# Kernel optimization log

Hardware: AMD Instinct MI355X
Metric: run time of the kernel (lower is better)

Reference implementation:

```python
import jax, jax.numpy as jnp
import numpy as np

B, T, D, H, E, K = 4, 2048, 512, 1024, 8, 2


def setup_inputs() -> dict:
    key = jax.random.key(0)
    ks = jax.random.split(key, 6)
    x = jax.random.normal(ks[0], (B, T, D), dtype=jnp.float32)
    Wg = jax.random.normal(ks[1], (D, E), dtype=jnp.float32) / np.sqrt(D)  # gate (no bias)
    W1 = jax.random.normal(ks[2], (E, D, H), dtype=jnp.float32) / np.sqrt(D)
    b1 = jnp.zeros((E, H), dtype=jnp.float32)
    W2 = jax.random.normal(ks[3], (E, H, D), dtype=jnp.float32) / np.sqrt(H)
    b2 = jnp.zeros((E, D), dtype=jnp.float32)
    return {"x": x, "Wg": Wg, "W1": W1, "b1": b1, "W2": W2, "b2": b2}


def reference(x, Wg, W1, b1, W2, b2):
    # Dropout is identity at inference (p applied only in train mode).
    Bx, Tx, Dx = x.shape
    N = Bx * Tx
    xf = x.reshape(N, Dx)

    # --- Router: top-k over gate logits, softmax over the k selected logits ---
    router_logits = xf @ Wg                               # [N, E]
    topk_logits, topk_idx = jax.lax.top_k(router_logits, K)  # [N, K]
    topk_w = jax.nn.softmax(topk_logits, axis=-1)         # [N, K]

    # Dense combine weights: combine[n, e] = sum of topk weights routing token n to expert e
    combine = jnp.zeros((N, E), dtype=x.dtype).at[
        jnp.arange(N)[:, None], topk_idx
    ].add(topk_w)                                         # [N, E]

    # --- Experts (batched over E): GELU(x W1 + b1) W2 + b2 ---
    h = jax.nn.gelu(jnp.einsum('nd,edh->enh', xf, W1) + b1[:, None, :],
                    approximate=False)                    # [E, N, H]
    y = jnp.einsum('enh,ehd->end', h, W2) + b2[:, None, :]  # [E, N, D]

    # --- Combine: weighted sum of expert outputs per token ---
    out = jnp.einsum('end,ne->nd', y, combine).reshape(Bx, Tx, Dx)

    aux_logits = router_logits.reshape(Bx, Tx, E)
    aux_idx = topk_idx.reshape(Bx, Tx, K)
    aux_w = topk_w.reshape(Bx, Tx, K)
    return out, aux_logits, aux_idx, aux_w
```

## Files before the change

### kernel.cpp

```cpp
#include <hip/hip_runtime.h>
#include <hip/hip_bf16.h>

#define NTOK 8192
#define DDIM 512
#define HDIM 1024
#define NEXP 8
#define TOPK 2

typedef __attribute__((ext_vector_type(8))) short short8;
typedef __attribute__((ext_vector_type(4))) float f32x4;

__device__ __forceinline__ short f2bf(float f) {
  union { float f; unsigned u; } v; v.f = f;
  unsigned r = v.u + 0x7fffu + ((v.u >> 16) & 1u);
  return (short)(r >> 16);
}
__device__ __forceinline__ float bf2f(short s) {
  union { unsigned u; float f; } v; v.u = ((unsigned)(unsigned short)s) << 16;
  return v.f;
}

__device__ __forceinline__ void async_lds16(const void* g, void* l) {
  __builtin_amdgcn_global_load_lds(
      (const __attribute__((address_space(1))) unsigned int*)g,
      (__attribute__((address_space(3))) unsigned int*)l,
      16, 0, 0);
}

__device__ __forceinline__ float gelu_f(float v) {
  float u2 = v * v;
  float z = v * (-1.5957691216f - 0.0713548163f * u2);
  float t = __expf(z);
  return v * __builtin_amdgcn_rcpf(1.f + t);
}

__global__ __launch_bounds__(256) void prep_kernel(
    const float* __restrict__ w1, short* __restrict__ w1t,
    const float* __restrict__ w2, short* __restrict__ w2t,
    const float* __restrict__ x, const float* __restrict__ wg,
    float* __restrict__ out_logits, float* __restrict__ out_idx,
    float* __restrict__ out_w, short* __restrict__ xb, int* __restrict__ counts) {
  __shared__ float tile[32][33];
  int raw = blockIdx.x;
  if (raw < 8192) {
    int z = raw >> 9;
    int tile_id = raw & 511;
    int R = (z < 8) ? DDIM : HDIM;
    int C = (z < 8) ? HDIM : DDIM;
    const float* s = ((z < 8) ? w1 : w2) + (size_t)(z & 7) * DDIM * HDIM;
    short* d = ((z < 8) ? w1t : w2t) + (size_t)(z & 7) * DDIM * HDIM;
    int tc = (z < 8) ? (tile_id & 31) : (tile_id & 15);
    int tr = (z < 8) ? (tile_id >> 5) : (tile_id >> 4);
    int c0 = tc * 32, r0 = tr * 32;
    int tx = threadIdx.x & 31, ty = threadIdx.x >> 5;
#pragma unroll
    for (int i = 0; i < 4; ++i)
      tile[ty + i * 8][tx] = s[(size_t)(r0 + ty + i * 8) * C + c0 + tx];
    __syncthreads();
#pragma unroll
    for (int i = 0; i < 4; ++i)
      d[(size_t)(c0 + ty + i * 8) * R + r0 + tx] = f2bf(tile[tx][ty + i * 8]);
    return;
  }
  int rb = raw - 8192;
  if (rb == 0 && threadIdx.x < NEXP) counts[threadIdx.x] = 0;
  int wave = threadIdx.x >> 6;
  int lane = threadIdx.x & 63;
  int n = rb * 4 + wave;

  const float* xrow = x + (size_t)n * DDIM;
  const float4* xv = (const float4*)xrow;
  float4 xa = xv[lane * 2], xbv = xv[lane * 2 + 1];
  float xs[8] = {xa.x, xa.y, xa.z, xa.w, xbv.x, xbv.y, xbv.z, xbv.w};

  short8 xc;
#pragma unroll
  for (int j = 0; j < 8; ++j) xc[j] = f2bf(xs[j]);
  *(short8*)(xb + (size_t)n * DDIM + lane * 8) = xc;

  float acc[8] = {0, 0, 0, 0, 0, 0, 0, 0};
#pragma unroll
  for (int j = 0; j < 8; ++j) {
    const float4* wr = (const float4*)(wg + (size_t)(lane * 8 + j) * NEXP);
    float4 w0 = wr[0], w1v = wr[1];
    float xj = xs[j];
    acc[0] += xj * w0.x; acc[1] += xj * w0.y; acc[2] += xj * w0.z; acc[3] += xj * w0.w;
    acc[4] += xj * w1v.x; acc[5] += xj * w1v.y; acc[6] += xj * w1v.z; acc[7] += xj * w1v.w;
  }
#pragma unroll
  for (int m = 32; m >= 1; m >>= 1) {
#pragma unroll
    for (int e = 0; e < 8; ++e) acc[e] += __shfl_xor(acc[e], m);
  }
  if (lane == 0) {
#pragma unroll
    for (int e = 0; e < 8; ++e) out_logits[(size_t)n * NEXP + e] = acc[e];
    int i1 = 0; float v1 = acc[0];
#pragma unroll
    for (int e = 1; e < 8; ++e) if (acc[e] > v1) { v1 = acc[e]; i1 = e; }
    int i2 = -1; float v2 = -3.4e38f;
#pragma unroll
    for (int e = 0; e < 8; ++e) if (e != i1 && acc[e] > v2) { v2 = acc[e]; i2 = e; }
    float ex = expf(v2 - v1);
    float s = 1.f / (1.f + ex);
    out_idx[n * 2] = (float)i1; out_idx[n * 2 + 1] = (float)i2;
    out_w[n * 2] = s; out_w[n * 2 + 1] = ex * s;
  }
}

__global__ __launch_bounds__(512) void build_lists(
    const float* __restrict__ idxf,
    int* __restrict__ counts, int* __restrict__ tok_list, int* __restrict__ slot_enc) {
  int t = blockIdx.x * 512 + threadIdx.x;
  int lane = threadIdx.x & 63;
  float2 iv = *(const float2*)(idxf + (size_t)t * 2);
  int es[2] = {(int)iv.x, (int)iv.y};
#pragma unroll
  for (int s = 0; s < 2; ++s) {
    int e = es[s];
#pragma unroll
    for (int ex = 0; ex < NEXP; ++ex) {
      unsigned long long m = __ballot(e == ex);
      if (e == ex) {
        int leader = __ffsll(m) - 1;
        int base = 0;
        if (lane == leader) base = atomicAdd(&counts[ex], __popcll(m));
        base = __shfl(base, leader);
        int rank = __popcll(m & ((1ull << lane) - 1ull));
        tok_list[ex * NTOK + base + rank] = t;
        slot_enc[t * 2 + s] = (ex << 16) | (base + rank);
      }
    }
  }
}

__global__ __launch_bounds__(256) void expert_gemm1(
    const short* __restrict__ xb, const short* __restrict__ w1t,
    const float* __restrict__ b1, short* __restrict__ hbuf,
    const int* __restrict__ ctrl, const int* __restrict__ tok_list) {
  int raw = blockIdx.x;
  int bid = (raw & 7) * 512 + (raw >> 3);
  int e = bid >> 9;
  int rem = bid & 511;
  int mt = rem >> 3;
  int nt = rem & 7;
  int ce = ctrl[e];
  int m0 = mt * 128;
  if (m0 >= ce) return;
  int offe = 0;
#pragma unroll
  for (int i = 0; i < NEXP; ++i) offe += (i < e) ? ctrl[i] : 0;

  __shared__ char smem[34816];

  int tid = threadIdx.x;
  int wave = tid >> 6;
  int lane = tid & 63;

  int sr = tid >> 2;
  int kc = (((tid & 3) ^ ((sr >> 1) & 3)) * 8);
  int ia = m0 + sr;      if (ia >= ce) ia = ce - 1;
  int ib = m0 + sr + 64; if (ib >= ce) ib = ce - 1;
  const short* gA0 = xb + (size_t)tok_list[e * NTOK + ia] * DDIM + kc;
  const short* gA1 = xb + (size_t)tok_list[e * NTOK + ib] * DDIM + kc;
  const short* gB0 = w1t + ((size_t)e * HDIM + nt * 128 + sr) * DDIM + kc;
  const short* gB1 = gB0 + (size_t)64 * DDIM;

  f32x4 acc[4][4];
#pragma unroll
  for (int i = 0; i < 4; ++i)
#pragma unroll
    for (int j = 0; j < 4; ++j) acc[i][j] = (f32x4){0.f, 0.f, 0.f, 0.f};

  int wm = (wave >> 1) * 64;
  int wn = (wave & 1) * 64;
  int lr = lane & 15;
  int kswz = ((lane >> 4) * 8) ^ (((lr >> 1) & 3) << 3);

  int colb = nt * 128 + wn;
  float bb[4];
#pragma unroll
  for (int j = 0; j < 4; ++j) bb[j] = b1[e * HDIM + colb + j * 16 + lr];

#define STAGE1(t) do {                                                  \
    int _k = (t) * 32;                                                  \
    char* _lA = smem + (((t) & 1) << 14) + wave * 1024;                 \
    char* _lB = _lA + 8192;                                             \
    async_lds16(gA0 + _k, _lA); async_lds16(gA1 + _k, _lA + 4096);      \
    async_lds16(gB0 + _k, _lB); async_lds16(gB1 + _k, _lB + 4096);      \
  } while (0)

  STAGE1(0);
#pragma unroll
  for (int t = 0; t < 16; ++t) {
    asm volatile("s_waitcnt vmcnt(0)\n\ts_barrier" ::: "memory");
    if (t + 1 < 16) STAGE1(t + 1);
    const short* As = (const short*)(smem + ((t & 1) << 14));
    const short* Bs = As + 4096;
    short8 a[4], b[4];
#pragma unroll
    for (int i = 0; i < 4; ++i) a[i] = *(const short8*)&As[(wm + i * 16 + lr) * 32 + kswz];
#pragma unroll
    for (int j = 0; j < 4; ++j) b[j] = *(const short8*)&Bs[(wn + j * 16 + lr) * 32 + kswz];
    __builtin_amdgcn_s_setprio(1);
#pragma unroll
    for (int i = 0; i < 4; ++i)
#pragma unroll
      for (int j = 0; j < 4; ++j)
        acc[i][j] = __builtin_amdgcn_mfma_f32_16x16x32_bf16(a[i], b[j], acc[i][j], 0, 0, 0);
    __builtin_amdgcn_s_setprio(0);
    asm volatile("s_waitcnt lgkmcnt(0)" ::: "memory");
  }
#undef STAGE1
  __syncthreads();

  short* ep = (short*)(smem + wave * 8704);
#pragma unroll
  for (int j = 0; j < 4; ++j) {
#pragma unroll
    for (int i = 0; i < 4; ++i) {
#pragma unroll
      for (int q = 0; q < 4; ++q) {
        int rl = i * 16 + (lane >> 4) * 4 + q;
        ep[rl * 68 + j * 16 + lr] = f2bf(gelu_f(acc[i][j][q] + bb[j]));
      }
    }
  }
  __syncthreads();
#pragma unroll
  for (int s = 0; s < 8; ++s) {
    int idx = s * 64 + lane;
    int rl = idx >> 3;
    int c8 = (idx & 7) * 8;
    int gidx = m0 + wm + rl;
    if (gidx < ce) {
      *(short8*)&hbuf[(size_t)(offe + gidx) * HDIM + colb + c8] = *(short8*)&ep[rl * 68 + c8];
    }
  }
}

__global__ __launch_bounds__(256) void expert_gemm2(
    const short* __restrict__ hbuf, const short* __restrict__ w2t,
    const float* __restrict__ b2, short* __restrict__ ybuf,
    const int* __restrict__ ctrl) {
  int raw = blockIdx.x;
  int bid = (raw & 7) * 256 + (raw >> 3);
  int e = bid >> 8;
  int rem = bid & 255;
  int mt = rem >> 2;
  int nt = rem & 3;
  int ce = ctrl[e];
  int m0 = mt * 128;
  if (m0 >= ce) return;
  int offe = 0;
#pragma unroll
  for (int i = 0; i < NEXP; ++i) offe += (i < e) ? ctrl[i] : 0;

  __shared__ char smem[34816];

  int tid = threadIdx.x;
  int wave = tid >> 6;
  int lane = tid & 63;

  int sr = tid >> 2;
  int kc = (((tid & 3) ^ ((sr >> 1) & 3)) * 8);
  int ia = m0 + sr;      if (ia >= ce) ia = ce - 1;
  int ib = m0 + sr + 64; if (ib >= ce) ib = ce - 1;
  const short* gA0 = hbuf + (size_t)(offe + ia) * HDIM + kc;
  const short* gA1 = hbuf + (size_t)(offe + ib) * HDIM + kc;
  const short* gB0 = w2t + ((size_t)e * DDIM + nt * 128 + sr) * HDIM + kc;
  const short* gB1 = gB0 + (size_t)64 * HDIM;

  f32x4 acc[4][4];
#pragma unroll
  for (int i = 0; i < 4; ++i)
#pragma unroll
    for (int j = 0; j < 4; ++j) acc[i][j] = (f32x4){0.f, 0.f, 0.f, 0.f};

  int wm = (wave >> 1) * 64;
  int wn = (wave & 1) * 64;
  int lr = lane & 15;
  int kswz = ((lane >> 4) * 8) ^ (((lr >> 1) & 3) << 3);

  int colb = nt * 128 + wn;
  float bb[4];
#pragma unroll
  for (int j = 0; j < 4; ++j) bb[j] = b2[e * DDIM + colb + j * 16 + lr];

#define STAGE2(t) do {                                                  \
    int _k = (t) * 32;                                                  \
    char* _lA = smem + (((t) & 1) << 14) + wave * 1024;                 \
    char* _lB = _lA + 8192;                                             \
    async_lds16(gA0 + _k, _lA); async_lds16(gA1 + _k, _lA + 4096);      \
    async_lds16(gB0 + _k, _lB); async_lds16(gB1 + _k, _lB + 4096);      \
  } while (0)

  STAGE2(0);
#pragma unroll
  for (int t = 0; t < 32; ++t) {
    asm volatile("s_waitcnt vmcnt(0)\n\ts_barrier" ::: "memory");
    if (t + 1 < 32) STAGE2(t + 1);
    const short* As = (const short*)(smem + ((t & 1) << 14));
    const short* Bs = As + 4096;
    short8 a[4], b[4];
#pragma unroll
    for (int i = 0; i < 4; ++i) a[i] = *(const short8*)&As[(wm + i * 16 + lr) * 32 + kswz];
#pragma unroll
    for (int j = 0; j < 4; ++j) b[j] = *(const short8*)&Bs[(wn + j * 16 + lr) * 32 + kswz];
    __builtin_amdgcn_s_setprio(1);
#pragma unroll
    for (int i = 0; i < 4; ++i)
#pragma unroll
      for (int j = 0; j < 4; ++j)
        acc[i][j] = __builtin_amdgcn_mfma_f32_16x16x32_bf16(a[i], b[j], acc[i][j], 0, 0, 0);
    __builtin_amdgcn_s_setprio(0);
    asm volatile("s_waitcnt lgkmcnt(0)" ::: "memory");
  }
#undef STAGE2
  __syncthreads();

  short* ep = (short*)(smem + wave * 8704);
#pragma unroll
  for (int j = 0; j < 4; ++j) {
#pragma unroll
    for (int i = 0; i < 4; ++i) {
#pragma unroll
      for (int q = 0; q < 4; ++q) {
        int rl = i * 16 + (lane >> 4) * 4 + q;
        ep[rl * 68 + j * 16 + lr] = f2bf(acc[i][j][q] + bb[j]);
      }
    }
  }
  __syncthreads();
#pragma unroll
  for (int s = 0; s < 8; ++s) {
    int idx = s * 64 + lane;
    int rl = idx >> 3;
    int c8 = (idx & 7) * 8;
    int gidx = m0 + wm + rl;
    if (gidx < ce) {
      *(short8*)&ybuf[(size_t)(offe + gidx) * DDIM + colb + c8] = *(short8*)&ep[rl * 68 + c8];
    }
  }
}

__global__ __launch_bounds__(256) void combine_kernel(
    const short* __restrict__ ybuf, const int* __restrict__ slot_enc,
    const float* __restrict__ wf, const int* __restrict__ ctrl,
    float* __restrict__ out) {
  int wave = threadIdx.x >> 6;
  int lane = threadIdx.x & 63;
  int n = blockIdx.x * 4 + wave;
  int s0 = slot_enc[n * 2], s1 = slot_enc[n * 2 + 1];
  float w0 = wf[n * 2], w1 = wf[n * 2 + 1];
  int e0 = s0 >> 16, e1 = s1 >> 16;
  int off0 = 0, off1 = 0;
#pragma unroll
  for (int i = 0; i < NEXP; ++i) {
    int c = ctrl[i];
    off0 += (i < e0) ? c : 0;
    off1 += (i < e1) ? c : 0;
  }
  int r0 = off0 + (s0 & 0xffff);
  int r1 = off1 + (s1 & 0xffff);
  short8 a = *(const short8*)&ybuf[(size_t)r0 * DDIM + lane * 8];
  short8 b = *(const short8*)&ybuf[(size_t)r1 * DDIM + lane * 8];
  float r[8];
#pragma unroll
  for (int k = 0; k < 8; ++k) r[k] = w0 * bf2f(a[k]) + w1 * bf2f(b[k]);
  float4 o0 = {r[0], r[1], r[2], r[3]};
  float4 o1 = {r[4], r[5], r[6], r[7]};
  *(float4*)&out[(size_t)n * DDIM + lane * 8] = o0;
  *(float4*)&out[(size_t)n * DDIM + lane * 8 + 4] = o1;
}

extern "C" void kernel_launch(void* const* d_in, const int* in_sizes, int n_in,
                              void* d_out, int out_size, void* d_ws, size_t ws_size,
                              hipStream_t stream) {
  const float* x  = (const float*)d_in[0];
  const float* wg = (const float*)d_in[1];
  const float* w1 = (const float*)d_in[2];
  const float* b1 = (const float*)d_in[3];
  const float* w2 = (const float*)d_in[4];
  const float* b2 = (const float*)d_in[5];
  float* out = (float*)d_out;

  char* ws = (char*)d_ws;
  int*   ctrl = (int*)ws;
  int*   tok  = (int*)(ws + 1024);
  int*   slot = (int*)(ws + 263168);
  short* xb   = (short*)(ws + 328704);
  short* w1t  = (short*)(ws + 8717312);
  short* w2t  = (short*)(ws + 17105920);
  short* hb   = (short*)(ws + 25494528);
  short* yb   = (short*)(ws + 328704);

  float* out_logits = out + (size_t)NTOK * DDIM;
  float* out_idx = out_logits + (size_t)NTOK * NEXP;
  float* out_w = out_idx + (size_t)NTOK * TOPK;

  prep_kernel<<<10240, 256, 0, stream>>>(w1, w1t, w2, w2t, x, wg,
                                         out_logits, out_idx, out_w, xb, ctrl);
  build_lists<<<16, 512, 0, stream>>>(out_idx, ctrl, tok, slot);

  expert_gemm1<<<4096, 256, 0, stream>>>(xb, w1t, b1, hb, ctrl, tok);
  expert_gemm2<<<2048, 256, 0, stream>>>(hb, w2t, b2, yb, ctrl);
  combine_kernel<<<2048, 256, 0, stream>>>(yb, slot, out_w, ctrl, out);
}
```

Baseline: 123.4 us.

## Enlarge expert GEMM1 tile to 256x256 with 8 waves and interleaved load/MFMA pipeline

Rewrites the first expert GEMM to use 256x256 output tiles computed by 512-thread blocks, each wave holding a 128x64 accumulator, with a 64-wide K step and double-buffered LDS. Global-to-LDS loads are split into quarter-stages interleaved between MFMA groups under barriers and priority raises, in a ping-pong schedule. The goal is more data reuse per byte loaded and better overlap of memory with matrix work. The cost is higher register pressure, fewer blocks (more tail waste for small experts), a 64KB LDS footprint and an epilogue that now synchronizes four times. The LDS swizzle is also dropped, which may add bank conflicts.

```diff
diff --git a/kernel.cpp b/kernel.cpp
--- a/kernel.cpp
+++ b/kernel.cpp
@@ -134,108 +134,157 @@
   }
 }
 
-__global__ __launch_bounds__(256) void expert_gemm1(
+__global__ __launch_bounds__(512, 2) void expert_gemm1(
     const short* __restrict__ xb, const short* __restrict__ w1t,
     const float* __restrict__ b1, short* __restrict__ hbuf,
     const int* __restrict__ ctrl, const int* __restrict__ tok_list) {
   int raw = blockIdx.x;
-  int bid = (raw & 7) * 512 + (raw >> 3);
-  int e = bid >> 9;
-  int rem = bid & 511;
-  int mt = rem >> 3;
-  int nt = rem & 7;
+  int e = raw & 7;
+  int rem = raw >> 3;
+  int mt = rem >> 2;
+  int nt = rem & 3;
   int ce = ctrl[e];
-  int m0 = mt * 128;
+  int m0 = mt * 256;
   if (m0 >= ce) return;
   int offe = 0;
 #pragma unroll
   for (int i = 0; i < NEXP; ++i) offe += (i < e) ? ctrl[i] : 0;
 
-  __shared__ char smem[34816];
+  __shared__ char smem[65536];
 
   int tid = threadIdx.x;
-  int wave = tid >> 6;
+  int w = tid >> 6;
   int lane = tid & 63;
 
-  int sr = tid >> 2;
-  int kc = (((tid & 3) ^ ((sr >> 1) & 3)) * 8);
-  int ia = m0 + sr;      if (ia >= ce) ia = ce - 1;
-  int ib = m0 + sr + 64; if (ib >= ce) ib = ce - 1;
-  const short* gA0 = xb + (size_t)tok_list[e * NTOK + ia] * DDIM + kc;
-  const short* gA1 = xb + (size_t)tok_list[e * NTOK + ib] * DDIM + kc;
-  const short* gB0 = w1t + ((size_t)e * HDIM + nt * 128 + sr) * DDIM + kc;
-  const short* gB1 = gB0 + (size_t)64 * DDIM;
-
-  f32x4 acc[4][4];
-#pragma unroll
-  for (int i = 0; i < 4; ++i)
+  int srow = lane >> 2;
+  int schunk = lane & 3;
+  const short* aptr[2]; const short* bptr[2]; int adst[2];
+#pragma unroll
+  for (int h = 0; h < 2; ++h) {
+    int r = h * 128 + w * 16 + srow;
+    int ga = m0 + r; if (ga >= ce) ga = ce - 1;
+    aptr[h] = xb + (size_t)tok_list[e * NTOK + ga] * DDIM + schunk * 8;
+    bptr[h] = w1t + ((size_t)e * HDIM + nt * 256 + r) * DDIM + schunk * 8;
+    adst[h] = (h * 128 + w * 16) * 64;
+  }
+#define STGA(h, t, buf) async_lds16(aptr[h] + (t) * 32, smem + (buf) * 32768 + adst[h])
+#define STGB(h, t, buf) async_lds16(bptr[h] + (t) * 32, smem + (buf) * 32768 + 16384 + adst[h])
+
+  int wm = (w >> 2) * 128;
+  int wnq = (w & 3) * 64;
+  int lr = lane & 15;
+  int kh16 = (lane >> 4) * 16;
+#define RA(i_, base) (*(const short8*)((base) + (wm + (i_) * 16 + lr) * 64 + kh16))
+#define RB(j_, base) (*(const short8*)((base) + 16384 + (wnq + (j_) * 16 + lr) * 64 + kh16))
+
+  f32x4 acc[8][4];
+#pragma unroll
+  for (int i = 0; i < 8; ++i)
 #pragma unroll
     for (int j = 0; j < 4; ++j) acc[i][j] = (f32x4){0.f, 0.f, 0.f, 0.f};
 
-  int wm = (wave >> 1) * 64;
-  int wn = (wave & 1) * 64;
-  int lr = lane & 15;
-  int kswz = ((lane >> 4) * 8) ^ (((lr >> 1) & 3) << 3);
-
-  int colb = nt * 128 + wn;
+  int colb = nt * 256 + wnq;
   float bb[4];
 #pragma unroll
   for (int j = 0; j < 4; ++j) bb[j] = b1[e * HDIM + colb + j * 16 + lr];
 
-#define STAGE1(t) do {                                                  \
-    int _k = (t) * 32;                                                  \
-    char* _lA = smem + (((t) & 1) << 14) + wave * 1024;                 \
-    char* _lB = _lA + 8192;                                             \
-    async_lds16(gA0 + _k, _lA); async_lds16(gA1 + _k, _lA + 4096);      \
-    async_lds16(gB0 + _k, _lB); async_lds16(gB1 + _k, _lB + 4096);      \
+#define MFMA8(q, a0_, a1_)                                                          \
+  do {                                                                              \
+    acc[2*(q)][0]   = __builtin_amdgcn_mfma_f32_16x16x32_bf16(a0_, b0, acc[2*(q)][0],   0,0,0); \
+    acc[2*(q)][1]   = __builtin_amdgcn_mfma_f32_16x16x32_bf16(a0_, b1, acc[2*(q)][1],   0,0,0); \
+    acc[2*(q)][2]   = __builtin_amdgcn_mfma_f32_16x16x32_bf16(a0_, b2, acc[2*(q)][2],   0,0,0); \
+    acc[2*(q)][3]   = __builtin_amdgcn_mfma_f32_16x16x32_bf16(a0_, b3, acc[2*(q)][3],   0,0,0); \
+    acc[2*(q)+1][0] = __builtin_amdgcn_mfma_f32_16x16x32_bf16(a1_, b0, acc[2*(q)+1][0], 0,0,0); \
+    acc[2*(q)+1][1] = __builtin_amdgcn_mfma_f32_16x16x32_bf16(a1_, b1, acc[2*(q)+1][1], 0,0,0); \
+    acc[2*(q)+1][2] = __builtin_amdgcn_mfma_f32_16x16x32_bf16(a1_, b2, acc[2*(q)+1][2], 0,0,0); \
+    acc[2*(q)+1][3] = __builtin_amdgcn_mfma_f32_16x16x32_bf16(a1_, b3, acc[2*(q)+1][3], 0,0,0); \
   } while (0)
 
-  STAGE1(0);
-#pragma unroll
-  for (int t = 0; t < 16; ++t) {
-    asm volatile("s_waitcnt vmcnt(0)\n\ts_barrier" ::: "memory");
-    if (t + 1 < 16) STAGE1(t + 1);
-    const short* As = (const short*)(smem + ((t & 1) << 14));
-    const short* Bs = As + 4096;
-    short8 a[4], b[4];
-#pragma unroll
-    for (int i = 0; i < 4; ++i) a[i] = *(const short8*)&As[(wm + i * 16 + lr) * 32 + kswz];
-#pragma unroll
-    for (int j = 0; j < 4; ++j) b[j] = *(const short8*)&Bs[(wn + j * 16 + lr) * 32 + kswz];
-    __builtin_amdgcn_s_setprio(1);
-#pragma unroll
-    for (int i = 0; i < 4; ++i)
-#pragma unroll
-      for (int j = 0; j < 4; ++j)
-        acc[i][j] = __builtin_amdgcn_mfma_f32_16x16x32_bf16(a[i], b[j], acc[i][j], 0, 0, 0);
-    __builtin_amdgcn_s_setprio(0);
-    asm volatile("s_waitcnt lgkmcnt(0)" ::: "memory");
-  }
-#undef STAGE1
+#define SYNC_IN()                                              \
+  asm volatile("s_barrier" ::: "memory");                      \
+  asm volatile("s_waitcnt lgkmcnt(0)" ::: "memory");           \
+  __builtin_amdgcn_sched_barrier(0);                           \
+  __builtin_amdgcn_s_setprio(1)
+#define SYNC_OUT()                                             \
+  __builtin_amdgcn_s_setprio(0);                               \
+  asm volatile("s_barrier" ::: "memory")
+#define SYNC_OUT_DRAIN2()                                      \
+  __builtin_amdgcn_s_setprio(0);                               \
+  asm volatile("s_waitcnt vmcnt(2)\n\ts_barrier" ::: "memory")
+#define SYNC_OUT_DRAIN0()                                      \
+  __builtin_amdgcn_s_setprio(0);                               \
+  asm volatile("s_waitcnt vmcnt(0)\n\ts_barrier" ::: "memory")
+
+  STGB(0, 0, 0); STGB(1, 0, 0); STGA(0, 0, 0); STGA(1, 0, 0);
+  STGB(0, 1, 1); STGB(1, 1, 1);
+  asm volatile("s_waitcnt vmcnt(2)\n\ts_barrier" ::: "memory");
+
+  const char* BUF0 = smem;
+  const char* BUF1 = smem + 32768;
+#pragma unroll
+  for (int i = 0; i < 8; ++i) {
+    short8 b0, b1, b2, b3, a0, a1;
+    b0 = RB(0, BUF0); b1 = RB(1, BUF0); b2 = RB(2, BUF0); b3 = RB(3, BUF0);
+    a0 = RA(0, BUF0); a1 = RA(1, BUF0);
+    STGA(0, 2 * i + 1, 1);
+    SYNC_IN(); MFMA8(0, a0, a1); SYNC_OUT();
+    a0 = RA(2, BUF0); a1 = RA(3, BUF0);
+    STGA(1, 2 * i + 1, 1);
+    SYNC_IN(); MFMA8(1, a0, a1); SYNC_OUT();
+    a0 = RA(4, BUF0); a1 = RA(5, BUF0);
+    if (i < 7) STGB(0, 2 * i + 2, 0);
+    SYNC_IN(); MFMA8(2, a0, a1); SYNC_OUT();
+    a0 = RA(6, BUF0); a1 = RA(7, BUF0);
+    if (i < 7) STGB(1, 2 * i + 2, 0);
+    SYNC_IN(); MFMA8(3, a0, a1);
+    if (i < 7) { SYNC_OUT_DRAIN2(); } else { SYNC_OUT_DRAIN0(); }
+    b0 = RB(0, BUF1); b1 = RB(1, BUF1); b2 = RB(2, BUF1); b3 = RB(3, BUF1);
+    a0 = RA(0, BUF1); a1 = RA(1, BUF1);
+    if (i < 7) STGA(0, 2 * i + 2, 0);
+    SYNC_IN(); MFMA8(0, a0, a1); SYNC_OUT();
+    a0 = RA(2, BUF1); a1 = RA(3, BUF1);
+    if (i < 7) STGA(1, 2 * i + 2, 0);
+    SYNC_IN(); MFMA8(1, a0, a1); SYNC_OUT();
+    a0 = RA(4, BUF1); a1 = RA(5, BUF1);
+    if (i < 7) STGB(0, 2 * i + 3, 1);
+    SYNC_IN(); MFMA8(2, a0, a1); SYNC_OUT();
+    a0 = RA(6, BUF1); a1 = RA(7, BUF1);
+    if (i < 7) STGB(1, 2 * i + 3, 1);
+    SYNC_IN(); MFMA8(3, a0, a1);
+    if (i < 7) { SYNC_OUT_DRAIN2(); } else { SYNC_OUT_DRAIN0(); }
+  }
+#undef STGA
+#undef STGB
+#undef RA
+#undef RB
   __syncthreads();
 
-  short* ep = (short*)(smem + wave * 8704);
-#pragma unroll
-  for (int j = 0; j < 4; ++j) {
-#pragma unroll
-    for (int i = 0; i < 4; ++i) {
-#pragma unroll
-      for (int q = 0; q < 4; ++q) {
-        int rl = i * 16 + (lane >> 4) * 4 + q;
-        ep[rl * 68 + j * 16 + lr] = f2bf(gelu_f(acc[i][j][q] + bb[j]));
+  short* ep = (short*)(smem + w * 4352);
+#pragma unroll
+  for (int p = 0; p < 4; ++p) {
+#pragma unroll
+    for (int ii = 0; ii < 2; ++ii) {
+#pragma unroll
+      for (int j = 0; j < 4; ++j) {
+#pragma unroll
+        for (int q = 0; q < 4; ++q) {
+          int rl = ii * 16 + (lane >> 4) * 4 + q;
+          ep[rl * 68 + j * 16 + lr] = f2bf(gelu_f(acc[p * 2 + ii][j][q] + bb[j]));
+        }
       }
     }
-  }
-  __syncthreads();
-#pragma unroll
-  for (int s = 0; s < 8; ++s) {
-    int idx = s * 64 + lane;
-    int rl = idx >> 3;
-    int c8 = (idx & 7) * 8;
-    int gidx = m0 + wm + rl;
-    if (gidx < ce) {
-      *(short8*)&hbuf[(size_t)(offe + gidx) * HDIM + colb + c8] = *(short8*)&ep[rl * 68 + c8];
+    __syncthreads();
+#pragma unroll
+    for (int s = 0; s < 4; ++s) {
+      int idx = s * 64 + lane;
+      int rl = idx >> 3;
+      int c8 = (idx & 7) * 8;
+      int gidx = m0 + wm + p * 32 + rl;
+      if (gidx < ce) {
+        *(short8*)&hbuf[(size_t)(offe + gidx) * HDIM + colb + c8] = *(short8*)&ep[rl * 68 + c8];
+      }
     }
+    __syncthreads();
   }
 }
 
@@ -403,7 +452,7 @@
                                          out_logits, out_idx, out_w, xb, ctrl);
   build_lists<<<16, 512, 0, stream>>>(out_idx, ctrl, tok, slot);
 
-  expert_gemm1<<<4096, 256, 0, stream>>>(xb, w1t, b1, hb, ctrl, tok);
+  expert_gemm1<<<1024, 512, 0, stream>>>(xb, w1t, b1, hb, ctrl, tok);
   expert_gemm2<<<2048, 256, 0, stream>>>(hb, w2t, b2, yb, ctrl);
   combine_kernel<<<2048, 256, 0, stream>>>(yb, slot, out_w, ctrl, out);
 }
```

Measured after the change: 135.2 us. 1.1x slower.
